# Optimization experiments

Measured on AMD Instinct MI355X. Metric: run time of the kernel, lower is better.

Reference implementation:

```python
import jax, jax.numpy as jnp
import numpy as np

MASK_FRAC = 0.95  # fraction of zero-labeled attributes to drop per row


def setup_inputs() -> dict:
    key = jax.random.key(0)
    k1, k2 = jax.random.split(key)
    B, C = 8192, 1024
    scores = jax.random.normal(k1, (B, C), dtype=jnp.float32)
    attributes = jax.random.randint(k2, (B, C), 0, 2, dtype=jnp.int32)
    return {"scores": scores, "attributes": attributes}


def reference(scores, attributes):
    # scores: [B, C] float logits; attributes: [B, C] binary {0,1} labels
    B, C = scores.shape
    attrs = attributes.astype(scores.dtype)

    # Per-row: randomly zero out round(0.95 * n_zeros) of the zero-label
    # positions (without replacement). Vectorized: give each zero position a
    # uniform key, nonzero positions a sentinel > 1, rank within the row, and
    # drop the k smallest ranks (all of which are zero positions).
    is_zero = attrs == 0
    u = jax.random.uniform(jax.random.key(42), (B, C))
    u = jnp.where(is_zero, u, 2.0)
    ranks = jnp.argsort(jnp.argsort(u, axis=1), axis=1)  # [B, C] rank of each pos
    n_zero = is_zero.sum(axis=1)  # [B]
    k = jnp.round(n_zero.astype(jnp.float32) * MASK_FRAC).astype(jnp.int32)  # [B]
    loss_mask = jnp.where(ranks < k[:, None], 0.0, 1.0).astype(scores.dtype)

    # multilabel_soft_margin_loss with per-class weight, mean over classes,
    # then mean over batch (original sums per-row losses and divides by B).
    ls_pos = jax.nn.log_sigmoid(scores)
    ls_neg = jax.nn.log_sigmoid(-scores)
    per_elem = loss_mask * (attrs * ls_pos + (1.0 - attrs) * ls_neg)  # [B, C]
    per_row = -per_elem.mean(axis=1)  # [B]
    return per_row.mean()
```

## Files before the change

kernel.cpp:

```cpp
#include <hip/hip_runtime.h>
#include <stdint.h>

static constexpr int B_ROWS = 8192;
static constexpr int C_COLS = 1024;
static constexpr uint32_t HALF_N = 4194304u;
static constexpr int NPAIR = B_ROWS / 2;
static constexpr int MAIN_BLOCKS = NPAIR / 4;

__device__ __forceinline__ uint32_t rotl32(uint32_t x, int d) {
  return (x << d) | (x >> (32 - d));
}

__device__ __forceinline__ void threefry2x32_k42(uint32_t& x0, uint32_t& x1) {
  const uint32_t ks0 = 0u;
  const uint32_t ks1 = 42u;
  const uint32_t ks2 = 0u ^ 42u ^ 0x1BD11BDAu;
  x0 += ks0; x1 += ks1;
#define TF_R(r) { x0 += x1; x1 = rotl32(x1, (r)); x1 ^= x0; }
  TF_R(13) TF_R(15) TF_R(26) TF_R(6)
  x0 += ks1; x1 += ks2 + 1u;
  TF_R(17) TF_R(29) TF_R(16) TF_R(24)
  x0 += ks2; x1 += ks0 + 2u;
  TF_R(13) TF_R(15) TF_R(26) TF_R(6)
  x0 += ks0; x1 += ks1 + 3u;
  TF_R(17) TF_R(29) TF_R(16) TF_R(24)
  x0 += ks1; x1 += ks2 + 4u;
  TF_R(13) TF_R(15) TF_R(26) TF_R(6)
  x0 += ks2; x1 += ks0 + 5u;
#undef TF_R
}

__global__ __launch_bounds__(256) void attr_loss_main(
    const float* __restrict__ scores, const int* __restrict__ attrs,
    double* __restrict__ partials) {
  __shared__ int hist[4][256];
  __shared__ float wsumf[4];

  const int t = threadIdx.x;
  const int lane = t & 63;
  const int w = t >> 6;
  const int pair = blockIdx.x * 4 + w;
  const int r0 = pair, r1 = pair + NPAIR;

  uint32_t key0[16], key1[16];
  uint32_t zm0 = 0, zm1 = 0;

#pragma unroll
  for (int i = 0; i < 4; ++i) {
    const int col = i * 256 + lane * 4;
    const int4 a0 = *reinterpret_cast<const int4*>(attrs + (size_t)r0 * C_COLS + col);
    const int4 a1 = *reinterpret_cast<const int4*>(attrs + (size_t)r1 * C_COLS + col);
    zm0 |= (a0.x == 0 ? 1u : 0u) << (i * 4 + 0);
    zm0 |= (a0.y == 0 ? 1u : 0u) << (i * 4 + 1);
    zm0 |= (a0.z == 0 ? 1u : 0u) << (i * 4 + 2);
    zm0 |= (a0.w == 0 ? 1u : 0u) << (i * 4 + 3);
    zm1 |= (a1.x == 0 ? 1u : 0u) << (i * 4 + 0);
    zm1 |= (a1.y == 0 ? 1u : 0u) << (i * 4 + 1);
    zm1 |= (a1.z == 0 ? 1u : 0u) << (i * 4 + 2);
    zm1 |= (a1.w == 0 ? 1u : 0u) << (i * 4 + 3);
  }

#pragma unroll
  for (int i = 0; i < 4; ++i) {
#pragma unroll
    for (int j = 0; j < 4; ++j) {
      const int col = i * 256 + lane * 4 + j;
      uint32_t x0 = (uint32_t)(r0 * C_COLS + col);
      uint32_t x1 = x0 + HALF_N;
      threefry2x32_k42(x0, x1);
      const uint32_t cb = (uint32_t)col >> 1;
      key0[i * 4 + j] = (x0 & 0xFFFFFE00u) | cb;
      key1[i * 4 + j] = (x1 & 0xFFFFFE00u) | cb;
    }
  }

  float lsum = 0.f;

#pragma unroll
  for (int r = 0; r < 2; ++r) {
    const uint32_t* key = r ? key1 : key0;
    const uint32_t zm = r ? zm1 : zm0;
    const float* srow = scores + (size_t)(r ? r1 : r0) * C_COLS;
    int* h = hist[w];

    *reinterpret_cast<int4*>(h + lane * 4) = make_int4(0, 0, 0, 0);
    __syncthreads();
#pragma unroll
    for (int e = 0; e < 16; ++e) {
      if ((zm >> e) & 1u) atomicAdd(&h[key[e] >> 24], 1);
    }
    __syncthreads();
    const int4 hv = *reinterpret_cast<const int4*>(h + lane * 4);

    const int s0 = hv.x, s1 = s0 + hv.y, s2 = s1 + hv.z, s3 = s2 + hv.w;
    int incl = s3;
#pragma unroll
    for (int d = 1; d < 64; d <<= 1) {
      const int o = __shfl_up(incl, d, 64);
      if (lane >= d) incl += o;
    }
    const int excl = incl - s3;
    const int n_zero = __shfl(incl, 63, 64);
    const int k = (int)rintf(0.95f * (float)n_zero);

    uint32_t T = 0u;
    if (k > 0) {
      const int target = k - 1;
      int myb = -1, myt = 0;
      const int ce0 = excl, ce1 = excl + s0, ce2 = excl + s1, ce3 = excl + s2;
      if (hv.x > 0 && ce0 <= target && target < ce0 + hv.x) { myb = lane * 4 + 0; myt = target - ce0; }
      if (hv.y > 0 && ce1 <= target && target < ce1 + hv.y) { myb = lane * 4 + 1; myt = target - ce1; }
      if (hv.z > 0 && ce2 <= target && target < ce2 + hv.z) { myb = lane * 4 + 2; myt = target - ce2; }
      if (hv.w > 0 && ce3 <= target && target < ce3 + hv.w) { myb = lane * 4 + 3; myt = target - ce3; }
      const unsigned long long bm = __ballot(myb >= 0);
      const int src = __ffsll((unsigned long long)bm) - 1;
      const uint32_t bucket = (uint32_t)__shfl(myb, src, 64);
      int tt = __shfl(myt, src, 64);

      uint32_t lowbar = 0u;
      while (true) {
        uint32_t mm = 0xFFFFFFFFu;
#pragma unroll
        for (int e = 0; e < 16; ++e) {
          const uint32_t kk = key[e];
          if (((zm >> e) & 1u) && (kk >> 24) == bucket && kk >= lowbar)
            mm = mm < kk ? mm : kk;
        }
#pragma unroll
        for (int d = 32; d >= 1; d >>= 1) {
          const uint32_t o = (uint32_t)__shfl_xor((int)mm, d, 64);
          mm = mm < o ? mm : o;
        }
        int c = 0;
#pragma unroll
        for (int e = 0; e < 16; ++e)
          c += (((zm >> e) & 1u) && key[e] == mm) ? 1 : 0;
#pragma unroll
        for (int d = 32; d >= 1; d >>= 1) c += __shfl_xor(c, d, 64);
        if (tt < c) { T = mm; break; }
        tt -= c;
        lowbar = mm + 1u;
      }
    }

#pragma unroll
    for (int i = 0; i < 4; ++i) {
      const float4 sv = *reinterpret_cast<const float4*>(srow + i * 256 + lane * 4);
      const float ss[4] = {sv.x, sv.y, sv.z, sv.w};
#pragma unroll
      for (int j = 0; j < 4; ++j) {
        const int e = i * 4 + j;
        const float s = ss[j];
        const float cmn = __logf(1.f + __expf(-fabsf(s)));
        if ((zm >> e) & 1u) {
          if (k <= 0 || key[e] > T) lsum += fminf(-s, 0.f) - cmn;
        } else {
          lsum += fminf(s, 0.f) - cmn;
        }
      }
    }
    __syncthreads();
  }

#pragma unroll
  for (int d = 32; d >= 1; d >>= 1) lsum += __shfl_xor(lsum, d, 64);
  if (lane == 0) wsumf[w] = lsum;
  __syncthreads();
  if (t == 0) {
    partials[blockIdx.x] =
        (double)wsumf[0] + (double)wsumf[1] + (double)wsumf[2] + (double)wsumf[3];
  }
}

__global__ __launch_bounds__(256) void finalize_kernel(
    const double* __restrict__ partials, float* __restrict__ out) {
  __shared__ double wred[4];
  const int t = threadIdx.x;
  const int lane = t & 63;
  const int w = t >> 6;
  double s = partials[t] + partials[t + 256] + partials[t + 512] + partials[t + 768];
#pragma unroll
  for (int d = 32; d >= 1; d >>= 1) s += __shfl_xor(s, d, 64);
  if (lane == 0) wred[w] = s;
  __syncthreads();
  if (t == 0) {
    const double tot = wred[0] + wred[1] + wred[2] + wred[3];
    out[0] = (float)(-tot / ((double)B_ROWS * (double)C_COLS));
  }
}

extern "C" void kernel_launch(void* const* d_in, const int* in_sizes, int n_in,
                              void* d_out, int out_size, void* d_ws, size_t ws_size,
                              hipStream_t stream) {
  const float* scores = (const float*)d_in[0];
  const int* attrs = (const int*)d_in[1];
  float* out = (float*)d_out;
  double* partials = (double*)d_ws;

  attr_loss_main<<<MAIN_BLOCKS, 256, 0, stream>>>(scores, attrs, partials);
  finalize_kernel<<<1, 256, 0, stream>>>(partials, out);
}
```

Baseline: 118.2 us.

## Use one-wave blocks, prefetch all row data, and fold the finalize kernel into atomics

```diff
diff --git a/kernel.cpp b/kernel.cpp
--- a/kernel.cpp
+++ b/kernel.cpp
@@ -5,7 +5,6 @@
 static constexpr int C_COLS = 1024;
 static constexpr uint32_t HALF_N = 4194304u;
 static constexpr int NPAIR = B_ROWS / 2;
-static constexpr int MAIN_BLOCKS = NPAIR / 4;
 
 __device__ __forceinline__ uint32_t rotl32(uint32_t x, int d) {
   return (x << d) | (x >> (32 - d));
@@ -30,68 +29,70 @@
 #undef TF_R
 }
 
-__global__ __launch_bounds__(256) void attr_loss_main(
+__global__ __launch_bounds__(64) void attr_loss_main(
     const float* __restrict__ scores, const int* __restrict__ attrs,
-    double* __restrict__ partials) {
-  __shared__ int hist[4][256];
-  __shared__ float wsumf[4];
+    float* __restrict__ out) {
+  __shared__ int hist[2][256];
 
-  const int t = threadIdx.x;
-  const int lane = t & 63;
-  const int w = t >> 6;
-  const int pair = blockIdx.x * 4 + w;
-  const int r0 = pair, r1 = pair + NPAIR;
+  const int lane = threadIdx.x;
+  const int pair = blockIdx.x;
+  const size_t base0 = (size_t)pair * C_COLS;
+  const size_t base1 = (size_t)(pair + NPAIR) * C_COLS;
 
-  uint32_t key0[16], key1[16];
-  uint32_t zm0 = 0, zm1 = 0;
-
+  float4 sv[2][4];
+  int4 av[2][4];
 #pragma unroll
   for (int i = 0; i < 4; ++i) {
     const int col = i * 256 + lane * 4;
-    const int4 a0 = *reinterpret_cast<const int4*>(attrs + (size_t)r0 * C_COLS + col);
-    const int4 a1 = *reinterpret_cast<const int4*>(attrs + (size_t)r1 * C_COLS + col);
-    zm0 |= (a0.x == 0 ? 1u : 0u) << (i * 4 + 0);
-    zm0 |= (a0.y == 0 ? 1u : 0u) << (i * 4 + 1);
-    zm0 |= (a0.z == 0 ? 1u : 0u) << (i * 4 + 2);
-    zm0 |= (a0.w == 0 ? 1u : 0u) << (i * 4 + 3);
-    zm1 |= (a1.x == 0 ? 1u : 0u) << (i * 4 + 0);
-    zm1 |= (a1.y == 0 ? 1u : 0u) << (i * 4 + 1);
-    zm1 |= (a1.z == 0 ? 1u : 0u) << (i * 4 + 2);
-    zm1 |= (a1.w == 0 ? 1u : 0u) << (i * 4 + 3);
+    sv[0][i] = *reinterpret_cast<const float4*>(scores + base0 + col);
+    sv[1][i] = *reinterpret_cast<const float4*>(scores + base1 + col);
+    av[0][i] = *reinterpret_cast<const int4*>(attrs + base0 + col);
+    av[1][i] = *reinterpret_cast<const int4*>(attrs + base1 + col);
   }
 
+  *reinterpret_cast<int4*>(&hist[0][lane * 4]) = make_int4(0, 0, 0, 0);
+  *reinterpret_cast<int4*>(&hist[1][lane * 4]) = make_int4(0, 0, 0, 0);
+
+  uint32_t key[2][16];
 #pragma unroll
   for (int i = 0; i < 4; ++i) {
 #pragma unroll
     for (int j = 0; j < 4; ++j) {
       const int col = i * 256 + lane * 4 + j;
-      uint32_t x0 = (uint32_t)(r0 * C_COLS + col);
+      uint32_t x0 = (uint32_t)(pair * C_COLS + col);
       uint32_t x1 = x0 + HALF_N;
       threefry2x32_k42(x0, x1);
       const uint32_t cb = (uint32_t)col >> 1;
-      key0[i * 4 + j] = (x0 & 0xFFFFFE00u) | cb;
-      key1[i * 4 + j] = (x1 & 0xFFFFFE00u) | cb;
+      key[0][i * 4 + j] = (x0 & 0xFFFFFE00u) | cb;
+      key[1][i * 4 + j] = (x1 & 0xFFFFFE00u) | cb;
     }
   }
 
-  float lsum = 0.f;
+  uint32_t zm[2] = {0u, 0u};
+#pragma unroll
+  for (int r = 0; r < 2; ++r) {
+#pragma unroll
+    for (int i = 0; i < 4; ++i) {
+      zm[r] |= (av[r][i].x == 0 ? 1u : 0u) << (i * 4 + 0);
+      zm[r] |= (av[r][i].y == 0 ? 1u : 0u) << (i * 4 + 1);
+      zm[r] |= (av[r][i].z == 0 ? 1u : 0u) << (i * 4 + 2);
+      zm[r] |= (av[r][i].w == 0 ? 1u : 0u) << (i * 4 + 3);
+    }
+  }
 
 #pragma unroll
   for (int r = 0; r < 2; ++r) {
-    const uint32_t* key = r ? key1 : key0;
-    const uint32_t zm = r ? zm1 : zm0;
-    const float* srow = scores + (size_t)(r ? r1 : r0) * C_COLS;
-    int* h = hist[w];
-
-    *reinterpret_cast<int4*>(h + lane * 4) = make_int4(0, 0, 0, 0);
-    __syncthreads();
 #pragma unroll
     for (int e = 0; e < 16; ++e) {
-      if ((zm >> e) & 1u) atomicAdd(&h[key[e] >> 24], 1);
+      if ((zm[r] >> e) & 1u) atomicAdd(&hist[r][key[r][e] >> 24], 1);
     }
-    __syncthreads();
-    const int4 hv = *reinterpret_cast<const int4*>(h + lane * 4);
+  }
 
+  int kk[2];
+  uint32_t T[2];
+#pragma unroll
+  for (int r = 0; r < 2; ++r) {
+    const int4 hv = *reinterpret_cast<const int4*>(&hist[r][lane * 4]);
     const int s0 = hv.x, s1 = s0 + hv.y, s2 = s1 + hv.z, s3 = s2 + hv.w;
     int incl = s3;
 #pragma unroll
@@ -102,8 +103,8 @@
     const int excl = incl - s3;
     const int n_zero = __shfl(incl, 63, 64);
     const int k = (int)rintf(0.95f * (float)n_zero);
-
-    uint32_t T = 0u;
+    kk[r] = k;
+    T[r] = 0u;
     if (k > 0) {
       const int target = k - 1;
       int myb = -1, myt = 0;
@@ -113,7 +114,7 @@
       if (hv.z > 0 && ce2 <= target && target < ce2 + hv.z) { myb = lane * 4 + 2; myt = target - ce2; }
       if (hv.w > 0 && ce3 <= target && target < ce3 + hv.w) { myb = lane * 4 + 3; myt = target - ce3; }
       const unsigned long long bm = __ballot(myb >= 0);
-      const int src = __ffsll((unsigned long long)bm) - 1;
+      const int src = __ffsll(bm) - 1;
       const uint32_t bucket = (uint32_t)__shfl(myb, src, 64);
       int tt = __shfl(myt, src, 64);
 
@@ -122,9 +123,9 @@
         uint32_t mm = 0xFFFFFFFFu;
 #pragma unroll
         for (int e = 0; e < 16; ++e) {
-          const uint32_t kk = key[e];
-          if (((zm >> e) & 1u) && (kk >> 24) == bucket && kk >= lowbar)
-            mm = mm < kk ? mm : kk;
+          const uint32_t kv = key[r][e];
+          if (((zm[r] >> e) & 1u) && (kv >> 24) == bucket && kv >= lowbar)
+            mm = mm < kv ? mm : kv;
         }
 #pragma unroll
         for (int d = 32; d >= 1; d >>= 1) {
@@ -134,58 +135,40 @@
         int c = 0;
 #pragma unroll
         for (int e = 0; e < 16; ++e)
-          c += (((zm >> e) & 1u) && key[e] == mm) ? 1 : 0;
+          c += (((zm[r] >> e) & 1u) && key[r][e] == mm) ? 1 : 0;
 #pragma unroll
         for (int d = 32; d >= 1; d >>= 1) c += __shfl_xor(c, d, 64);
-        if (tt < c) { T = mm; break; }
+        if (tt < c) { T[r] = mm; break; }
         tt -= c;
         lowbar = mm + 1u;
       }
     }
+  }
 
+  float lsum = 0.f;
+#pragma unroll
+  for (int r = 0; r < 2; ++r) {
 #pragma unroll
     for (int i = 0; i < 4; ++i) {
-      const float4 sv = *reinterpret_cast<const float4*>(srow + i * 256 + lane * 4);
-      const float ss[4] = {sv.x, sv.y, sv.z, sv.w};
+      const float ss[4] = {sv[r][i].x, sv[r][i].y, sv[r][i].z, sv[r][i].w};
 #pragma unroll
       for (int j = 0; j < 4; ++j) {
         const int e = i * 4 + j;
         const float s = ss[j];
         const float cmn = __logf(1.f + __expf(-fabsf(s)));
-        if ((zm >> e) & 1u) {
-          if (k <= 0 || key[e] > T) lsum += fminf(-s, 0.f) - cmn;
+        if ((zm[r] >> e) & 1u) {
+          if (kk[r] <= 0 || key[r][e] > T[r]) lsum += fminf(-s, 0.f) - cmn;
         } else {
           lsum += fminf(s, 0.f) - cmn;
         }
       }
     }
-    __syncthreads();
   }
 
 #pragma unroll
   for (int d = 32; d >= 1; d >>= 1) lsum += __shfl_xor(lsum, d, 64);
-  if (lane == 0) wsumf[w] = lsum;
-  __syncthreads();
-  if (t == 0) {
-    partials[blockIdx.x] =
-        (double)wsumf[0] + (double)wsumf[1] + (double)wsumf[2] + (double)wsumf[3];
-  }
-}
-
-__global__ __launch_bounds__(256) void finalize_kernel(
-    const double* __restrict__ partials, float* __restrict__ out) {
-  __shared__ double wred[4];
-  const int t = threadIdx.x;
-  const int lane = t & 63;
-  const int w = t >> 6;
-  double s = partials[t] + partials[t + 256] + partials[t + 512] + partials[t + 768];
-#pragma unroll
-  for (int d = 32; d >= 1; d >>= 1) s += __shfl_xor(s, d, 64);
-  if (lane == 0) wred[w] = s;
-  __syncthreads();
-  if (t == 0) {
-    const double tot = wred[0] + wred[1] + wred[2] + wred[3];
-    out[0] = (float)(-tot / ((double)B_ROWS * (double)C_COLS));
+  if (lane == 0) {
+    atomicAdd(out, lsum * (-1.0f / 8388608.0f));
   }
 }
 
@@ -195,8 +178,7 @@
   const float* scores = (const float*)d_in[0];
   const int* attrs = (const int*)d_in[1];
   float* out = (float*)d_out;
-  double* partials = (double*)d_ws;
 
-  attr_loss_main<<<MAIN_BLOCKS, 256, 0, stream>>>(scores, attrs, partials);
-  finalize_kernel<<<1, 256, 0, stream>>>(partials, out);
+  hipMemsetAsync(d_out, 0, sizeof(float), stream);
+  attr_loss_main<<<NPAIR, 64, 0, stream>>>(scores, attrs, out);
 }
```

Result: slower. 154.8 us (+31.0%).

## Split Threefry pair work across two wavefronts sharing keys via LDS

Applied to the files above, without the earlier changes.

```diff
diff --git a/kernel.cpp b/kernel.cpp
--- a/kernel.cpp
+++ b/kernel.cpp
@@ -5,7 +5,6 @@
 static constexpr int C_COLS = 1024;
 static constexpr uint32_t HALF_N = 4194304u;
 static constexpr int NPAIR = B_ROWS / 2;
-static constexpr int MAIN_BLOCKS = NPAIR / 4;
 
 __device__ __forceinline__ uint32_t rotl32(uint32_t x, int d) {
   return (x << d) | (x >> (32 - d));
@@ -30,155 +29,146 @@
 #undef TF_R
 }
 
-__global__ __launch_bounds__(256) void attr_loss_main(
+__global__ __launch_bounds__(128) void attr_loss_main(
     const float* __restrict__ scores, const int* __restrict__ attrs,
-    double* __restrict__ partials) {
-  __shared__ int hist[4][256];
-  __shared__ float wsumf[4];
+    float* __restrict__ partials) {
+  __shared__ int hist[2][256];
+  __shared__ uint32_t xbuf[2][512];
 
   const int t = threadIdx.x;
   const int lane = t & 63;
   const int w = t >> 6;
-  const int pair = blockIdx.x * 4 + w;
-  const int r0 = pair, r1 = pair + NPAIR;
+  const int pair = blockIdx.x;
+  const int myrow = pair + w * NPAIR;
+  const int selfc0 = w * 512 + lane * 8;
+  const int othc0 = (1 - w) * 512 + lane * 8;
 
-  uint32_t key0[16], key1[16];
-  uint32_t zm0 = 0, zm1 = 0;
+  int4 a0 = *reinterpret_cast<const int4*>(attrs + (size_t)myrow * C_COLS + selfc0);
+  int4 a1 = *reinterpret_cast<const int4*>(attrs + (size_t)myrow * C_COLS + selfc0 + 4);
+  int4 a2 = *reinterpret_cast<const int4*>(attrs + (size_t)myrow * C_COLS + othc0);
+  int4 a3 = *reinterpret_cast<const int4*>(attrs + (size_t)myrow * C_COLS + othc0 + 4);
+
+  *reinterpret_cast<int4*>(&hist[w][lane * 4]) = make_int4(0, 0, 0, 0);
+
+  uint32_t key[16];
+#pragma unroll
+  for (int j = 0; j < 8; ++j) {
+    const int col = selfc0 + j;
+    uint32_t x0 = (uint32_t)(pair * C_COLS + col);
+    uint32_t x1 = x0 + HALF_N;
+    threefry2x32_k42(x0, x1);
+    const uint32_t cb = (uint32_t)col >> 1;
+    const uint32_t k0 = (x0 & 0xFFFFFE00u) | cb;
+    const uint32_t k1 = (x1 & 0xFFFFFE00u) | cb;
+    key[j] = w ? k1 : k0;
+    xbuf[w][j * 64 + lane] = w ? k0 : k1;
+  }
+  __syncthreads();
+#pragma unroll
+  for (int j = 0; j < 8; ++j) {
+    key[8 + j] = xbuf[1 - w][j * 64 + lane];
+  }
+
+  uint32_t zm = 0u;
+  zm |= (a0.x == 0 ? 1u : 0u) << 0;  zm |= (a0.y == 0 ? 1u : 0u) << 1;
+  zm |= (a0.z == 0 ? 1u : 0u) << 2;  zm |= (a0.w == 0 ? 1u : 0u) << 3;
+  zm |= (a1.x == 0 ? 1u : 0u) << 4;  zm |= (a1.y == 0 ? 1u : 0u) << 5;
+  zm |= (a1.z == 0 ? 1u : 0u) << 6;  zm |= (a1.w == 0 ? 1u : 0u) << 7;
+  zm |= (a2.x == 0 ? 1u : 0u) << 8;  zm |= (a2.y == 0 ? 1u : 0u) << 9;
+  zm |= (a2.z == 0 ? 1u : 0u) << 10; zm |= (a2.w == 0 ? 1u : 0u) << 11;
+  zm |= (a3.x == 0 ? 1u : 0u) << 12; zm |= (a3.y == 0 ? 1u : 0u) << 13;
+  zm |= (a3.z == 0 ? 1u : 0u) << 14; zm |= (a3.w == 0 ? 1u : 0u) << 15;
 
 #pragma unroll
-  for (int i = 0; i < 4; ++i) {
-    const int col = i * 256 + lane * 4;
-    const int4 a0 = *reinterpret_cast<const int4*>(attrs + (size_t)r0 * C_COLS + col);
-    const int4 a1 = *reinterpret_cast<const int4*>(attrs + (size_t)r1 * C_COLS + col);
-    zm0 |= (a0.x == 0 ? 1u : 0u) << (i * 4 + 0);
-    zm0 |= (a0.y == 0 ? 1u : 0u) << (i * 4 + 1);
-    zm0 |= (a0.z == 0 ? 1u : 0u) << (i * 4 + 2);
-    zm0 |= (a0.w == 0 ? 1u : 0u) << (i * 4 + 3);
-    zm1 |= (a1.x == 0 ? 1u : 0u) << (i * 4 + 0);
-    zm1 |= (a1.y == 0 ? 1u : 0u) << (i * 4 + 1);
-    zm1 |= (a1.z == 0 ? 1u : 0u) << (i * 4 + 2);
-    zm1 |= (a1.w == 0 ? 1u : 0u) << (i * 4 + 3);
+  for (int e = 0; e < 16; ++e) {
+    if ((zm >> e) & 1u) atomicAdd(&hist[w][key[e] >> 24], 1);
   }
 
+  const float4 s0 = *reinterpret_cast<const float4*>(scores + (size_t)myrow * C_COLS + selfc0);
+  const float4 s1 = *reinterpret_cast<const float4*>(scores + (size_t)myrow * C_COLS + selfc0 + 4);
+  const float4 s2 = *reinterpret_cast<const float4*>(scores + (size_t)myrow * C_COLS + othc0);
+  const float4 s3 = *reinterpret_cast<const float4*>(scores + (size_t)myrow * C_COLS + othc0 + 4);
+
+  const int4 hv = *reinterpret_cast<const int4*>(&hist[w][lane * 4]);
+  const int c0 = hv.x, c1 = c0 + hv.y, c2 = c1 + hv.z, c3 = c2 + hv.w;
+  int incl = c3;
 #pragma unroll
-  for (int i = 0; i < 4; ++i) {
+  for (int d = 1; d < 64; d <<= 1) {
+    const int o = __shfl_up(incl, d, 64);
+    if (lane >= d) incl += o;
+  }
+  const int excl = incl - c3;
+  const int n_zero = __shfl(incl, 63, 64);
+  const int k = (int)rintf(0.95f * (float)n_zero);
+
+  uint32_t T = 0u;
+  if (k > 0) {
+    const int target = k - 1;
+    int myb = -1, myt = 0;
+    const int ce0 = excl, ce1 = excl + c0, ce2 = excl + c1, ce3 = excl + c2;
+    if (hv.x > 0 && ce0 <= target && target < ce0 + hv.x) { myb = lane * 4 + 0; myt = target - ce0; }
+    if (hv.y > 0 && ce1 <= target && target < ce1 + hv.y) { myb = lane * 4 + 1; myt = target - ce1; }
+    if (hv.z > 0 && ce2 <= target && target < ce2 + hv.z) { myb = lane * 4 + 2; myt = target - ce2; }
+    if (hv.w > 0 && ce3 <= target && target < ce3 + hv.w) { myb = lane * 4 + 3; myt = target - ce3; }
+    const unsigned long long bm = __ballot(myb >= 0);
+    const int src = __ffsll(bm) - 1;
+    const uint32_t bucket = (uint32_t)__shfl(myb, src, 64);
+    int tt = __shfl(myt, src, 64);
+
+    uint32_t lowbar = 0u;
+    while (true) {
+      uint32_t mm = 0xFFFFFFFFu;
 #pragma unroll
-    for (int j = 0; j < 4; ++j) {
-      const int col = i * 256 + lane * 4 + j;
-      uint32_t x0 = (uint32_t)(r0 * C_COLS + col);
-      uint32_t x1 = x0 + HALF_N;
-      threefry2x32_k42(x0, x1);
-      const uint32_t cb = (uint32_t)col >> 1;
-      key0[i * 4 + j] = (x0 & 0xFFFFFE00u) | cb;
-      key1[i * 4 + j] = (x1 & 0xFFFFFE00u) | cb;
+      for (int e = 0; e < 16; ++e) {
+        const uint32_t kv = key[e];
+        if (((zm >> e) & 1u) && (kv >> 24) == bucket && kv >= lowbar)
+          mm = mm < kv ? mm : kv;
+      }
+#pragma unroll
+      for (int d = 32; d >= 1; d >>= 1) {
+        const uint32_t o = (uint32_t)__shfl_xor((int)mm, d, 64);
+        mm = mm < o ? mm : o;
+      }
+      int c = 0;
+#pragma unroll
+      for (int e = 0; e < 16; ++e)
+        c += (((zm >> e) & 1u) && key[e] == mm) ? 1 : 0;
+#pragma unroll
+      for (int d = 32; d >= 1; d >>= 1) c += __shfl_xor(c, d, 64);
+      if (tt < c) { T = mm; break; }
+      tt -= c;
+      lowbar = mm + 1u;
     }
   }
 
   float lsum = 0.f;
-
+  const float ss[16] = {s0.x, s0.y, s0.z, s0.w, s1.x, s1.y, s1.z, s1.w,
+                        s2.x, s2.y, s2.z, s2.w, s3.x, s3.y, s3.z, s3.w};
 #pragma unroll
-  for (int r = 0; r < 2; ++r) {
-    const uint32_t* key = r ? key1 : key0;
-    const uint32_t zm = r ? zm1 : zm0;
-    const float* srow = scores + (size_t)(r ? r1 : r0) * C_COLS;
-    int* h = hist[w];
-
-    *reinterpret_cast<int4*>(h + lane * 4) = make_int4(0, 0, 0, 0);
-    __syncthreads();
-#pragma unroll
-    for (int e = 0; e < 16; ++e) {
-      if ((zm >> e) & 1u) atomicAdd(&h[key[e] >> 24], 1);
+  for (int e = 0; e < 16; ++e) {
+    const float s = ss[e];
+    const float cmn = __logf(1.f + __expf(-fabsf(s)));
+    if ((zm >> e) & 1u) {
+      if (k <= 0 || key[e] > T) lsum += fminf(-s, 0.f) - cmn;
+    } else {
+      lsum += fminf(s, 0.f) - cmn;
     }
-    __syncthreads();
-    const int4 hv = *reinterpret_cast<const int4*>(h + lane * 4);
-
-    const int s0 = hv.x, s1 = s0 + hv.y, s2 = s1 + hv.z, s3 = s2 + hv.w;
-    int incl = s3;
-#pragma unroll
-    for (int d = 1; d < 64; d <<= 1) {
-      const int o = __shfl_up(incl, d, 64);
-      if (lane >= d) incl += o;
-    }
-    const int excl = incl - s3;
-    const int n_zero = __shfl(incl, 63, 64);
-    const int k = (int)rintf(0.95f * (float)n_zero);
-
-    uint32_t T = 0u;
-    if (k > 0) {
-      const int target = k - 1;
-      int myb = -1, myt = 0;
-      const int ce0 = excl, ce1 = excl + s0, ce2 = excl + s1, ce3 = excl + s2;
-      if (hv.x > 0 && ce0 <= target && target < ce0 + hv.x) { myb = lane * 4 + 0; myt = target - ce0; }
-      if (hv.y > 0 && ce1 <= target && target < ce1 + hv.y) { myb = lane * 4 + 1; myt = target - ce1; }
-      if (hv.z > 0 && ce2 <= target && target < ce2 + hv.z) { myb = lane * 4 + 2; myt = target - ce2; }
-      if (hv.w > 0 && ce3 <= target && target < ce3 + hv.w) { myb = lane * 4 + 3; myt = target - ce3; }
-      const unsigned long long bm = __ballot(myb >= 0);
-      const int src = __ffsll((unsigned long long)bm) - 1;
-      const uint32_t bucket = (uint32_t)__shfl(myb, src, 64);
-      int tt = __shfl(myt, src, 64);
-
-      uint32_t lowbar = 0u;
-      while (true) {
-        uint32_t mm = 0xFFFFFFFFu;
-#pragma unroll
-        for (int e = 0; e < 16; ++e) {
-          const uint32_t kk = key[e];
-          if (((zm >> e) & 1u) && (kk >> 24) == bucket && kk >= lowbar)
-            mm = mm < kk ? mm : kk;
-        }
-#pragma unroll
-        for (int d = 32; d >= 1; d >>= 1) {
-          const uint32_t o = (uint32_t)__shfl_xor((int)mm, d, 64);
-          mm = mm < o ? mm : o;
-        }
-        int c = 0;
-#pragma unroll
-        for (int e = 0; e < 16; ++e)
-          c += (((zm >> e) & 1u) && key[e] == mm) ? 1 : 0;
-#pragma unroll
-        for (int d = 32; d >= 1; d >>= 1) c += __shfl_xor(c, d, 64);
-        if (tt < c) { T = mm; break; }
-        tt -= c;
-        lowbar = mm + 1u;
-      }
-    }
-
-#pragma unroll
-    for (int i = 0; i < 4; ++i) {
-      const float4 sv = *reinterpret_cast<const float4*>(srow + i * 256 + lane * 4);
-      const float ss[4] = {sv.x, sv.y, sv.z, sv.w};
-#pragma unroll
-      for (int j = 0; j < 4; ++j) {
-        const int e = i * 4 + j;
-        const float s = ss[j];
-        const float cmn = __logf(1.f + __expf(-fabsf(s)));
-        if ((zm >> e) & 1u) {
-          if (k <= 0 || key[e] > T) lsum += fminf(-s, 0.f) - cmn;
-        } else {
-          lsum += fminf(s, 0.f) - cmn;
-        }
-      }
-    }
-    __syncthreads();
   }
 
 #pragma unroll
   for (int d = 32; d >= 1; d >>= 1) lsum += __shfl_xor(lsum, d, 64);
-  if (lane == 0) wsumf[w] = lsum;
-  __syncthreads();
-  if (t == 0) {
-    partials[blockIdx.x] =
-        (double)wsumf[0] + (double)wsumf[1] + (double)wsumf[2] + (double)wsumf[3];
-  }
+  if (lane == 0) partials[blockIdx.x * 2 + w] = lsum;
 }
 
 __global__ __launch_bounds__(256) void finalize_kernel(
-    const double* __restrict__ partials, float* __restrict__ out) {
+    const float* __restrict__ partials, float* __restrict__ out) {
   __shared__ double wred[4];
   const int t = threadIdx.x;
   const int lane = t & 63;
   const int w = t >> 6;
-  double s = partials[t] + partials[t + 256] + partials[t + 512] + partials[t + 768];
+  double s = 0.0;
+#pragma unroll
+  for (int i = 0; i < 32; ++i) s += (double)partials[t + i * 256];
 #pragma unroll
   for (int d = 32; d >= 1; d >>= 1) s += __shfl_xor(s, d, 64);
   if (lane == 0) wred[w] = s;
@@ -195,8 +185,8 @@
   const float* scores = (const float*)d_in[0];
   const int* attrs = (const int*)d_in[1];
   float* out = (float*)d_out;
-  double* partials = (double*)d_ws;
+  float* partials = (float*)d_ws;
 
-  attr_loss_main<<<MAIN_BLOCKS, 256, 0, stream>>>(scores, attrs, partials);
+  attr_loss_main<<<NPAIR, 128, 0, stream>>>(scores, attrs, partials);
   finalize_kernel<<<1, 256, 0, stream>>>(partials, out);
 }
```

Measured after the change: 106.0 us. 1.12x faster.
